# Optimization experiments

Measured on AMD Instinct MI355X. Metric: run time of the kernel, lower is better.

## Reference

```python
import jax, jax.numpy as jnp
import numpy as np

B, F, V, D_EMB = 16384, 32, 50000, 16
D_IN = F * D_EMB            # 512, concat embedding dim
N_TASK, N_SPEC, N_SH = 2, 2, 2
E = N_TASK * N_SPEC + N_SH  # 6 experts per CGC level
H1, H2 = 512, 256           # expert_params dims
T1, T2 = 128, 64            # tower dims


def setup_inputs() -> dict:
    key = jax.random.key(0)
    ks = iter(jax.random.split(key, 32))
    def w(shape, s=0.05):
        return jax.random.normal(next(ks), shape, jnp.float32) * s
    return dict(
        x_ids=jax.random.randint(next(ks), (B, F), 0, V),
        emb=w((F, V, D_EMB)),
        e1_W1=w((E, D_IN, H1)), e1_b1=jnp.zeros((E, H1), jnp.float32),
        e1_W2=w((E, H1, H2)), e1_b2=jnp.zeros((E, H2), jnp.float32),
        g1_Ws=w((N_TASK, D_IN, N_SPEC + N_SH)), g1_bs=jnp.zeros((N_TASK, N_SPEC + N_SH), jnp.float32),
        g1_Wsh=w((D_IN, E)), g1_bsh=jnp.zeros((E,), jnp.float32),
        e2_W1=w((E, H2, H1)), e2_b1=jnp.zeros((E, H1), jnp.float32),
        e2_W2=w((E, H1, H2)), e2_b2=jnp.zeros((E, H2), jnp.float32),
        g2_Ws=w((N_TASK, H2, N_SPEC + N_SH)), g2_bs=jnp.zeros((N_TASK, N_SPEC + N_SH), jnp.float32),
        tw_W1=w((N_TASK, H2, T1)), tw_b1=jnp.zeros((N_TASK, T1), jnp.float32),
        tw_W2=w((N_TASK, T1, T2)), tw_b2=jnp.zeros((N_TASK, T2), jnp.float32),
    )


def _cgc(x_list, W1, b1, W2, b2, Wg, bg, Wg_sh=None, bg_sh=None):
    # Stack expert inputs: task-t specific experts read x_list[t], shared read x_list[-1].
    X = jnp.stack([x_list[0]] * N_SPEC + [x_list[1]] * N_SPEC + [x_list[-1]] * N_SH)  # [E,B,Din]
    # Grouped two-layer expert MLP (BatchNorm is identity at eval-mode init).
    h = jax.nn.relu(jnp.einsum('ebd,edh->ebh', X, W1) + b1[:, None, :])   # [E,B,H1]
    out = jax.nn.relu(jnp.einsum('ebh,eho->ebo', h, W2) + b2[:, None, :])  # [E,B,H2]
    outs = []
    for t in range(N_TASK):
        gate = jax.nn.softmax(x_list[t] @ Wg[t] + bg[t], axis=-1)          # [B, N_SPEC+N_SH]
        sel = jnp.concatenate([out[t * N_SPEC:(t + 1) * N_SPEC], out[-N_SH:]], axis=0)
        outs.append(jnp.einsum('bk,kbo->bo', gate, sel))
    if Wg_sh is not None:  # shared gate only for levels < n_level
        gate = jax.nn.softmax(x_list[-1] @ Wg_sh + bg_sh, axis=-1)          # [B,E]
        outs.append(jnp.einsum('bk,kbo->bo', gate, out))
    return outs


def reference(x_ids, emb, e1_W1, e1_b1, e1_W2, e1_b2, g1_Ws, g1_bs, g1_Wsh, g1_bsh,
              e2_W1, e2_b1, e2_W2, e2_b2, g2_Ws, g2_bs, tw_W1, tw_b1, tw_W2, tw_b2):
    # Embedding lookup per sparse feature, then flatten (squeeze_dim=True).
    embed_x = emb[jnp.arange(F)[None, :], x_ids].reshape(B, D_IN)  # [B, 512]
    xs = [embed_x] * (N_TASK + 1)
    xs = _cgc(xs, e1_W1, e1_b1, e1_W2, e1_b2, g1_Ws, g1_bs, g1_Wsh, g1_bsh)  # level 1 -> 3 outs
    xs = _cgc(xs, e2_W1, e2_b1, e2_W2, e2_b2, g2_Ws, g2_bs)                  # level 2 -> 2 outs
    ys = []
    for t in range(N_TASK):
        h = jax.nn.relu(xs[t] @ tw_W1[t] + tw_b1[t])
        h = jax.nn.relu(h @ tw_W2[t] + tw_b2[t])
        ys.append(jax.nn.sigmoid(h))  # PredictionLayer('classification')
    return jnp.concatenate(ys, axis=1)  # [B, N_TASK*T2]
```

## Files before the change

### kernel.cpp

```cpp
#include <hip/hip_runtime.h>

typedef unsigned short u16;
typedef __attribute__((ext_vector_type(4))) unsigned short u16x4;
typedef __attribute__((ext_vector_type(8))) unsigned short u16x8;
typedef __attribute__((ext_vector_type(8))) short s16x8;
typedef __attribute__((ext_vector_type(4))) float f32x4;

#define BATCH 16384
#define NFEAT 32
#define NVOCAB 50000

__device__ __forceinline__ u16 f2bf(float f) {
    union { float f; unsigned u; } v; v.f = f;
    unsigned u = v.u;
    return (u16)((u + 0x7fffu + ((u >> 16) & 1u)) >> 16);
}
__device__ __forceinline__ float bf2f(u16 h) {
    union { unsigned u; float f; } v; v.u = ((unsigned)h) << 16;
    return v.f;
}

struct PrepDesc { const float* src; u16* dst; int K; int N; int nz; int zbase; };
struct PrepArgs { PrepDesc d[6]; };

__global__ void prep_weights(PrepArgs args) {
    int z = blockIdx.z;
    int di = 0;
    #pragma unroll
    for (int i = 0; i < 6; i++)
        if (z >= args.d[i].zbase && z < args.d[i].zbase + args.d[i].nz) di = i;
    PrepDesc d = args.d[di];
    int zz = z - d.zbase;
    int k0 = blockIdx.x * 32, n0 = blockIdx.y * 32;
    if (k0 >= d.K || n0 >= d.N) return;
    __shared__ float tile[32][33];
    const float* src = d.src + (long)zz * d.K * d.N;
    u16* dst = d.dst + (long)zz * d.K * d.N;
    int tx = threadIdx.x & 31, ty = threadIdx.x >> 5;
    for (int r = ty; r < 32; r += 8) {
        int k = k0 + r, n = n0 + tx;
        tile[r][tx] = (k < d.K && n < d.N) ? src[(long)k * d.N + n] : 0.f;
    }
    __syncthreads();
    for (int r = ty; r < 32; r += 8) {
        int n = n0 + r, k = k0 + tx;
        if (n < d.N && k < d.K) dst[(long)n * d.K + k] = f2bf(tile[tx][r]);
    }
}

__global__ void gather_embed(const int* __restrict__ ids,
                             const float* __restrict__ emb,
                             u16* __restrict__ out) {
    int idx = blockIdx.x * 256 + threadIdx.x;
    int d4 = idx & 3;
    int f  = (idx >> 2) & 31;
    int b  = idx >> 7;
    int id = ids[b * NFEAT + f];
    const float4* p = (const float4*)(emb + ((long)f * NVOCAB + id) * 16) + d4;
    float4 v = *p;
    u16x4 o;
    o.x = f2bf(v.x); o.y = f2bf(v.y); o.z = f2bf(v.z); o.w = f2bf(v.w);
    *(u16x4*)(out + (long)b * 512 + f * 16 + d4 * 4) = o;
}

template<int ACT, typename OUT_T>
__global__ __launch_bounds__(256, 2)
void gemm_bt(const u16* __restrict__ A, const u16* __restrict__ Bt,
             const float* __restrict__ bias, OUT_T* __restrict__ C,
             int M, int N, int K,
             long a_zstride, int a_zdiv, long c_zstride, int c_row_stride) {
    constexpr int LROW = 72;
    __shared__ u16 sA[128 * LROW];
    __shared__ u16 sB[128 * LROW];
    const int z = blockIdx.z;
    const u16* Ab = A + (long)(z / a_zdiv) * a_zstride;
    const u16* Bb = Bt + (long)z * N * K;
    const int m0 = blockIdx.x * 128;
    const int n0 = blockIdx.y * 128;
    const int tid = threadIdx.x;
    const int lane = tid & 63;
    const int w = tid >> 6;
    const int wm = (w & 1) * 64;
    const int wn = (w >> 1) * 64;
    const int l16 = lane & 15;
    const int q = lane >> 4;

    f32x4 acc[4][4] = {};

    for (int k0 = 0; k0 < K; k0 += 64) {
        u16x8 va[4], vb[4];
        #pragma unroll
        for (int i = 0; i < 4; i++) {
            int c = tid + i * 256;
            int row = c >> 3;
            int col = (c & 7) * 8;
            va[i] = *(const u16x8*)(Ab + (long)(m0 + row) * K + k0 + col);
            int nrow = n0 + row;
            if (nrow < N) vb[i] = *(const u16x8*)(Bb + (long)nrow * K + k0 + col);
            else          vb[i] = (u16x8)0;
        }
        __syncthreads();
        #pragma unroll
        for (int i = 0; i < 4; i++) {
            int c = tid + i * 256;
            int row = c >> 3;
            int col = (c & 7) * 8;
            *(u16x8*)(&sA[row * LROW + col]) = va[i];
            *(u16x8*)(&sB[row * LROW + col]) = vb[i];
        }
        __syncthreads();
        #pragma unroll
        for (int kk = 0; kk < 2; kk++) {
            s16x8 af[4], bfr[4];
            #pragma unroll
            for (int i = 0; i < 4; i++)
                af[i] = *(const s16x8*)(&sA[(wm + i * 16 + l16) * LROW + kk * 32 + q * 8]);
            #pragma unroll
            for (int i = 0; i < 4; i++)
                bfr[i] = *(const s16x8*)(&sB[(wn + i * 16 + l16) * LROW + kk * 32 + q * 8]);
            #pragma unroll
            for (int mt = 0; mt < 4; mt++)
                #pragma unroll
                for (int nt = 0; nt < 4; nt++)
                    acc[mt][nt] = __builtin_amdgcn_mfma_f32_16x16x32_bf16(
                        af[mt], bfr[nt], acc[mt][nt], 0, 0, 0);
        }
    }

    const float* bb = bias + (long)z * N;
    OUT_T* Cp = C + (long)z * c_zstride;
    #pragma unroll
    for (int nt = 0; nt < 4; nt++) {
        int gcol = n0 + wn + nt * 16 + l16;
        if (gcol >= N) continue;
        float bv = bb[gcol];
        #pragma unroll
        for (int mt = 0; mt < 4; mt++) {
            int grow = m0 + wm + mt * 16 + q * 4;
            #pragma unroll
            for (int r = 0; r < 4; r++) {
                float v = acc[mt][nt][r] + bv;
                if (ACT == 1) v = fmaxf(v, 0.f);
                else if (ACT == 2) v = 1.f / (1.f + __expf(-v));
                if constexpr (sizeof(OUT_T) == 2)
                    Cp[(long)(grow + r) * c_row_stride + gcol] = f2bf(v);
                else
                    Cp[(long)(grow + r) * c_row_stride + gcol] = v;
            }
        }
    }
}

__global__ void gate_combine1(const u16* __restrict__ embed,
                              const u16* __restrict__ out1,
                              const float* __restrict__ g1Ws, const float* __restrict__ g1bs,
                              const float* __restrict__ gWsh, const float* __restrict__ gbsh,
                              u16* __restrict__ x1) {
    int b = blockIdx.x;
    __shared__ float sgw[14];
    int tid = threadIdx.x, w = tid >> 6, lane = tid & 63;
    if (w < 3) {
        int ng = (w == 2) ? 6 : 4;
        const float* W = (w == 2) ? gWsh : (g1Ws + w * 512 * 4);
        const u16* xr = embed + (long)b * 512;
        float lg[6] = {0, 0, 0, 0, 0, 0};
        for (int e = lane; e < 512; e += 64) {
            float xv = bf2f(xr[e]);
            #pragma unroll
            for (int g = 0; g < 6; g++)
                if (g < ng) lg[g] += xv * W[e * ng + g];
        }
        #pragma unroll
        for (int g = 0; g < 6; g++) {
            float v = lg[g];
            for (int off = 32; off > 0; off >>= 1) v += __shfl_xor(v, off);
            lg[g] = v;
        }
        if (lane == 0) {
            const float* bs = (w == 2) ? gbsh : (g1bs + w * 4);
            float mx = -1e30f;
            for (int g = 0; g < ng; g++) { lg[g] += bs[g]; mx = fmaxf(mx, lg[g]); }
            float s = 0.f, ex[6];
            for (int g = 0; g < ng; g++) { ex[g] = __expf(lg[g] - mx); s += ex[g]; }
            int base = (w == 2) ? 8 : w * 4;
            for (int g = 0; g < ng; g++) sgw[base + g] = ex[g] / s;
        }
    }
    __syncthreads();
    int j = tid;
    const u16* ob = out1 + (long)b * 256 + j;
    float o[6];
    #pragma unroll
    for (int k = 0; k < 6; k++) o[k] = bf2f(ob[(long)k * BATCH * 256]);
    float v0 = sgw[0] * o[0] + sgw[1] * o[1] + sgw[2] * o[4] + sgw[3] * o[5];
    float v1 = sgw[4] * o[2] + sgw[5] * o[3] + sgw[6] * o[4] + sgw[7] * o[5];
    float v2 = 0.f;
    #pragma unroll
    for (int k = 0; k < 6; k++) v2 += sgw[8 + k] * o[k];
    x1[((long)0 * BATCH + b) * 256 + j] = f2bf(v0);
    x1[((long)1 * BATCH + b) * 256 + j] = f2bf(v1);
    x1[((long)2 * BATCH + b) * 256 + j] = f2bf(v2);
}

__global__ void gate_combine2(const u16* __restrict__ x1,
                              const u16* __restrict__ out2,
                              const float* __restrict__ g2Ws, const float* __restrict__ g2bs,
                              u16* __restrict__ x2) {
    int b = blockIdx.x;
    __shared__ float sgw[8];
    int tid = threadIdx.x, w = tid >> 6, lane = tid & 63;
    if (w < 2) {
        const float* W = g2Ws + w * 256 * 4;
        const u16* xr = x1 + ((long)w * BATCH + b) * 256;
        float lg[4] = {0, 0, 0, 0};
        for (int e = lane; e < 256; e += 64) {
            float xv = bf2f(xr[e]);
            #pragma unroll
            for (int g = 0; g < 4; g++) lg[g] += xv * W[e * 4 + g];
        }
        #pragma unroll
        for (int g = 0; g < 4; g++) {
            float v = lg[g];
            for (int off = 32; off > 0; off >>= 1) v += __shfl_xor(v, off);
            lg[g] = v;
        }
        if (lane == 0) {
            float mx = -1e30f;
            for (int g = 0; g < 4; g++) { lg[g] += g2bs[w * 4 + g]; mx = fmaxf(mx, lg[g]); }
            float s = 0.f, ex[4];
            for (int g = 0; g < 4; g++) { ex[g] = __expf(lg[g] - mx); s += ex[g]; }
            for (int g = 0; g < 4; g++) sgw[w * 4 + g] = ex[g] / s;
        }
    }
    __syncthreads();
    int j = tid;
    const u16* ob = out2 + (long)b * 256 + j;
    float o[6];
    #pragma unroll
    for (int k = 0; k < 6; k++) o[k] = bf2f(ob[(long)k * BATCH * 256]);
    float v0 = sgw[0] * o[0] + sgw[1] * o[1] + sgw[2] * o[4] + sgw[3] * o[5];
    float v1 = sgw[4] * o[2] + sgw[5] * o[3] + sgw[6] * o[4] + sgw[7] * o[5];
    x2[((long)0 * BATCH + b) * 256 + j] = f2bf(v0);
    x2[((long)1 * BATCH + b) * 256 + j] = f2bf(v1);
}

extern "C" void kernel_launch(void* const* d_in, const int* in_sizes, int n_in,
                              void* d_out, int out_size, void* d_ws, size_t ws_size,
                              hipStream_t stream) {
    const int*   x_ids = (const int*)  d_in[0];
    const float* emb   = (const float*)d_in[1];
    const float* e1W1  = (const float*)d_in[2];
    const float* e1b1  = (const float*)d_in[3];
    const float* e1W2  = (const float*)d_in[4];
    const float* e1b2  = (const float*)d_in[5];
    const float* g1Ws  = (const float*)d_in[6];
    const float* g1bs  = (const float*)d_in[7];
    const float* g1Wsh = (const float*)d_in[8];
    const float* g1bsh = (const float*)d_in[9];
    const float* e2W1  = (const float*)d_in[10];
    const float* e2b1  = (const float*)d_in[11];
    const float* e2W2  = (const float*)d_in[12];
    const float* e2b2  = (const float*)d_in[13];
    const float* g2Ws  = (const float*)d_in[14];
    const float* g2bs  = (const float*)d_in[15];
    const float* twW1  = (const float*)d_in[16];
    const float* twb1  = (const float*)d_in[17];
    const float* twW2  = (const float*)d_in[18];
    const float* twb2  = (const float*)d_in[19];
    float* out = (float*)d_out;

    char* ws = (char*)d_ws;
    u16* embed   = (u16*)(ws + 0);
    u16* wt_e1W1 = (u16*)(ws + 16777216);
    u16* wt_e1W2 = (u16*)(ws + 19922944);
    u16* wt_e2W1 = (u16*)(ws + 21495808);
    u16* wt_e2W2 = (u16*)(ws + 23068672);
    u16* wt_twW1 = (u16*)(ws + 24641536);
    u16* wt_twW2 = (u16*)(ws + 24772608);
    u16* h_buf   = (u16*)(ws + 24805376);
    u16* o_buf   = (u16*)(ws + 125468672);
    u16* x1      = (u16*)(ws + 175800320);
    u16* x2      = (u16*)(ws + 200966144);
    u16* th      = (u16*)(ws + 217743360);

    PrepArgs pa;
    pa.d[0] = { e1W1, wt_e1W1, 512, 512, 6,  0 };
    pa.d[1] = { e1W2, wt_e1W2, 512, 256, 6,  6 };
    pa.d[2] = { e2W1, wt_e2W1, 256, 512, 6, 12 };
    pa.d[3] = { e2W2, wt_e2W2, 512, 256, 6, 18 };
    pa.d[4] = { twW1, wt_twW1, 256, 128, 2, 24 };
    pa.d[5] = { twW2, wt_twW2, 128,  64, 2, 26 };
    prep_weights<<<dim3(16, 16, 28), 256, 0, stream>>>(pa);

    gather_embed<<<dim3(BATCH * NFEAT * 4 / 256), 256, 0, stream>>>(x_ids, emb, embed);

    gemm_bt<1, u16><<<dim3(128, 4, 6), 256, 0, stream>>>(
        embed, wt_e1W1, e1b1, h_buf, BATCH, 512, 512,
        0L, 1, (long)BATCH * 512, 512);
    gemm_bt<1, u16><<<dim3(128, 2, 6), 256, 0, stream>>>(
        h_buf, wt_e1W2, e1b2, o_buf, BATCH, 256, 512,
        (long)BATCH * 512, 1, (long)BATCH * 256, 256);

    gate_combine1<<<dim3(BATCH), 256, 0, stream>>>(embed, o_buf, g1Ws, g1bs, g1Wsh, g1bsh, x1);

    gemm_bt<1, u16><<<dim3(128, 4, 6), 256, 0, stream>>>(
        x1, wt_e2W1, e2b1, h_buf, BATCH, 512, 256,
        (long)BATCH * 256, 2, (long)BATCH * 512, 512);
    gemm_bt<1, u16><<<dim3(128, 2, 6), 256, 0, stream>>>(
        h_buf, wt_e2W2, e2b2, o_buf, BATCH, 256, 512,
        (long)BATCH * 512, 1, (long)BATCH * 256, 256);

    gate_combine2<<<dim3(BATCH), 256, 0, stream>>>(x1, o_buf, g2Ws, g2bs, x2);

    gemm_bt<1, u16><<<dim3(128, 1, 2), 256, 0, stream>>>(
        x2, wt_twW1, twb1, th, BATCH, 128, 256,
        (long)BATCH * 256, 1, (long)BATCH * 128, 128);
    gemm_bt<2, float><<<dim3(128, 1, 2), 256, 0, stream>>>(
        th, wt_twW2, twb2, out, BATCH, 64, 128,
        (long)BATCH * 128, 1, 64L, 128);
}
```

Measured before the change: 529.9 us.

## Load GEMM tiles directly to LDS with XOR swizzle and vectorized epilogue

The GEMM now fills shared memory with global_load_lds (direct global-to-LDS DMA) instead of staging through registers. The LDS padding is replaced by an XOR swizzle to avoid bank conflicts. The MFMA operands are swapped so each lane holds four consecutive columns, which lets the epilogue write vectorized 4-wide stores and load the bias as a float4. The N-bound check on B loads is dropped, so rows past N may be read out of bounds, and float4 bias loads assume aligned, in-range columns.

```diff
diff --git a/kernel.cpp b/kernel.cpp
--- a/kernel.cpp
+++ b/kernel.cpp
@@ -18,6 +18,12 @@
 __device__ __forceinline__ float bf2f(u16 h) {
     union { unsigned u; float f; } v; v.u = ((unsigned)h) << 16;
     return v.f;
+}
+
+__device__ __forceinline__ void load_lds16(const u16* g, u16* l) {
+    __builtin_amdgcn_global_load_lds(
+        (const __attribute__((address_space(1))) void*)g,
+        (__attribute__((address_space(3))) void*)l, 16, 0, 0);
 }
 
 struct PrepDesc { const float* src; u16* dst; int K; int N; int nz; int zbase; };
@@ -69,9 +75,8 @@
              const float* __restrict__ bias, OUT_T* __restrict__ C,
              int M, int N, int K,
              long a_zstride, int a_zdiv, long c_zstride, int c_row_stride) {
-    constexpr int LROW = 72;
-    __shared__ u16 sA[128 * LROW];
-    __shared__ u16 sB[128 * LROW];
+    __shared__ u16 sA[128 * 64];
+    __shared__ u16 sB[128 * 64];
     const int z = blockIdx.z;
     const u16* Ab = A + (long)(z / a_zdiv) * a_zstride;
     const u16* Bb = Bt + (long)z * N * K;
@@ -85,67 +90,80 @@
     const int l16 = lane & 15;
     const int q = lane >> 4;
 
+    const u16* gA[4];
+    const u16* gB[4];
+    u16* lA[4];
+    u16* lB[4];
+    #pragma unroll
+    for (int i = 0; i < 4; i++) {
+        int c = i * 256 + tid;
+        int row = c >> 3;
+        int lc = (c & 7) ^ (row & 7);
+        gA[i] = Ab + (long)(m0 + row) * K + lc * 8;
+        gB[i] = Bb + (long)(n0 + row) * K + lc * 8;
+        int cb = (i * 256 + (tid & ~63)) * 8;
+        lA[i] = &sA[cb];
+        lB[i] = &sB[cb];
+    }
+    const int key = l16 & 7;
+
     f32x4 acc[4][4] = {};
 
     for (int k0 = 0; k0 < K; k0 += 64) {
-        u16x8 va[4], vb[4];
-        #pragma unroll
-        for (int i = 0; i < 4; i++) {
-            int c = tid + i * 256;
-            int row = c >> 3;
-            int col = (c & 7) * 8;
-            va[i] = *(const u16x8*)(Ab + (long)(m0 + row) * K + k0 + col);
-            int nrow = n0 + row;
-            if (nrow < N) vb[i] = *(const u16x8*)(Bb + (long)nrow * K + k0 + col);
-            else          vb[i] = (u16x8)0;
-        }
-        __syncthreads();
-        #pragma unroll
-        for (int i = 0; i < 4; i++) {
-            int c = tid + i * 256;
-            int row = c >> 3;
-            int col = (c & 7) * 8;
-            *(u16x8*)(&sA[row * LROW + col]) = va[i];
-            *(u16x8*)(&sB[row * LROW + col]) = vb[i];
-        }
+        if (k0) __syncthreads();
+        #pragma unroll
+        for (int i = 0; i < 4; i++) load_lds16(gA[i] + k0, lA[i]);
+        #pragma unroll
+        for (int i = 0; i < 4; i++) load_lds16(gB[i] + k0, lB[i]);
         __syncthreads();
         #pragma unroll
         for (int kk = 0; kk < 2; kk++) {
             s16x8 af[4], bfr[4];
             #pragma unroll
-            for (int i = 0; i < 4; i++)
-                af[i] = *(const s16x8*)(&sA[(wm + i * 16 + l16) * LROW + kk * 32 + q * 8]);
-            #pragma unroll
-            for (int i = 0; i < 4; i++)
-                bfr[i] = *(const s16x8*)(&sB[(wn + i * 16 + l16) * LROW + kk * 32 + q * 8]);
+            for (int i = 0; i < 4; i++) {
+                int row = wm + i * 16 + l16;
+                int pc = ((kk << 2) | q) ^ key;
+                af[i] = *(const s16x8*)(&sA[row * 64 + pc * 8]);
+            }
+            #pragma unroll
+            for (int i = 0; i < 4; i++) {
+                int row = wn + i * 16 + l16;
+                int pc = ((kk << 2) | q) ^ key;
+                bfr[i] = *(const s16x8*)(&sB[row * 64 + pc * 8]);
+            }
             #pragma unroll
             for (int mt = 0; mt < 4; mt++)
                 #pragma unroll
                 for (int nt = 0; nt < 4; nt++)
                     acc[mt][nt] = __builtin_amdgcn_mfma_f32_16x16x32_bf16(
-                        af[mt], bfr[nt], acc[mt][nt], 0, 0, 0);
+                        bfr[nt], af[mt], acc[mt][nt], 0, 0, 0);
         }
     }
 
     const float* bb = bias + (long)z * N;
     OUT_T* Cp = C + (long)z * c_zstride;
     #pragma unroll
-    for (int nt = 0; nt < 4; nt++) {
-        int gcol = n0 + wn + nt * 16 + l16;
-        if (gcol >= N) continue;
-        float bv = bb[gcol];
-        #pragma unroll
-        for (int mt = 0; mt < 4; mt++) {
-            int grow = m0 + wm + mt * 16 + q * 4;
+    for (int mt = 0; mt < 4; mt++) {
+        int grow = m0 + wm + mt * 16 + l16;
+        OUT_T* rowp = Cp + (long)grow * c_row_stride;
+        #pragma unroll
+        for (int nt = 0; nt < 4; nt++) {
+            int gc = n0 + wn + nt * 16 + q * 4;
+            if (gc >= N) continue;
+            float4 bv = *(const float4*)(bb + gc);
+            f32x4 v = acc[mt][nt];
+            v.x += bv.x; v.y += bv.y; v.z += bv.z; v.w += bv.w;
             #pragma unroll
             for (int r = 0; r < 4; r++) {
-                float v = acc[mt][nt][r] + bv;
-                if (ACT == 1) v = fmaxf(v, 0.f);
-                else if (ACT == 2) v = 1.f / (1.f + __expf(-v));
-                if constexpr (sizeof(OUT_T) == 2)
-                    Cp[(long)(grow + r) * c_row_stride + gcol] = f2bf(v);
-                else
-                    Cp[(long)(grow + r) * c_row_stride + gcol] = v;
+                if (ACT == 1) v[r] = fmaxf(v[r], 0.f);
+                else if (ACT == 2) v[r] = 1.f / (1.f + __expf(-v[r]));
+            }
+            if constexpr (sizeof(OUT_T) == 2) {
+                u16x4 o;
+                o.x = f2bf(v.x); o.y = f2bf(v.y); o.z = f2bf(v.z); o.w = f2bf(v.w);
+                *(u16x4*)(rowp + gc) = o;
+            } else {
+                *(float4*)(rowp + gc) = *(float4*)&v;
             }
         }
     }
```

Result: no change. 534.1 us (+0.8%).
